# Kernel optimization log

Hardware: AMD Instinct MI355X
Metric: run time of the kernel (lower is better)

The kernel has to match this reference:

```python
import jax, jax.numpy as jnp
import numpy as np

N_NODES = 100000
N_EDGES = 1600000
IN_DIM = 128
HEADS = 8
NEG_SLOPE = 0.2  # PyG GATConv default


def _glorot(key, shape):
    fan_in, fan_out = shape[0], shape[-1]
    lim = jnp.sqrt(6.0 / (fan_in + fan_out))
    return jax.random.uniform(key, shape, jnp.float32, -lim, lim)


def setup_inputs() -> dict:
    key = jax.random.key(0)
    ks = jax.random.split(key, 20)
    x = jax.random.normal(ks[0], (N_NODES, IN_DIM), jnp.float32)
    edge_index = jax.random.randint(ks[1], (2, N_EDGES), 0, N_NODES, jnp.int32)
    # layer 1: 128 -> 8 heads x 16
    W1 = _glorot(ks[2], (128, 128)); a_src1 = _glorot(ks[3], (8, 16)); a_dst1 = _glorot(ks[4], (8, 16)); b1 = jnp.zeros((128,), jnp.float32)
    # layer 2: 128 -> 8 heads x 16
    W2 = _glorot(ks[5], (128, 128)); a_src2 = _glorot(ks[6], (8, 16)); a_dst2 = _glorot(ks[7], (8, 16)); b2 = jnp.zeros((128,), jnp.float32)
    # layer 3: 128 -> 1 head x 64, concat=False (mean)
    W3 = _glorot(ks[8], (128, 64)); a_src3 = _glorot(ks[9], (1, 64)); a_dst3 = _glorot(ks[10], (1, 64)); b3 = jnp.zeros((64,), jnp.float32)
    Wout = _glorot(ks[11], (64, 2)); bout = jnp.zeros((2,), jnp.float32)
    return {"x": x, "edge_index": edge_index,
            "W1": W1, "a_src1": a_src1, "a_dst1": a_dst1, "b1": b1,
            "W2": W2, "a_src2": a_src2, "a_dst2": a_dst2, "b2": b2,
            "W3": W3, "a_src3": a_src3, "a_dst3": a_dst3, "b3": b3,
            "Wout": Wout, "bout": bout}


def gat_conv(x, src, dst, W, a_src, a_dst, bias, concat):
    """PyG-style GATConv (eval mode, self-loops already appended to src/dst)."""
    n = x.shape[0]
    H, C = a_src.shape
    h = (x @ W).reshape(n, H, C)                        # [N,H,C]
    alpha_src = jnp.einsum('nhc,hc->nh', h, a_src)       # [N,H]
    alpha_dst = jnp.einsum('nhc,hc->nh', h, a_dst)       # [N,H]
    e = jax.nn.leaky_relu(alpha_src[src] + alpha_dst[dst], NEG_SLOPE)  # [E,H]
    # segment softmax over incoming edges of each destination node
    m = jax.ops.segment_max(e, dst, num_segments=n)      # [N,H]
    ex = jnp.exp(e - m[dst])
    denom = jax.ops.segment_sum(ex, dst, num_segments=n)  # [N,H]
    alpha = ex / (denom[dst] + 1e-16)                    # [E,H]
    # weighted gather-scatter aggregation
    msg = alpha[:, :, None] * h[src]                     # [E,H,C]
    out = jax.ops.segment_sum(msg, dst, num_segments=n)  # [N,H,C]
    out = out.reshape(n, H * C) if concat else out.mean(axis=1)
    return out + bias


def reference(x, edge_index, W1, a_src1, a_dst1, b1, W2, a_src2, a_dst2, b2,
              W3, a_src3, a_dst3, b3, Wout, bout):
    n = x.shape[0]
    loops = jnp.arange(n, dtype=edge_index.dtype)
    src = jnp.concatenate([edge_index[0], loops])
    dst = jnp.concatenate([edge_index[1], loops])
    h = jax.nn.elu(gat_conv(x, src, dst, W1, a_src1, a_dst1, b1, concat=True))
    h = jax.nn.elu(gat_conv(h, src, dst, W2, a_src2, a_dst2, b2, concat=True))
    h = jax.nn.elu(gat_conv(h, src, dst, W3, a_src3, a_dst3, b3, concat=False))
    return h @ Wout + bout
```

## Files before the change

### kernel.cpp

```cpp
#include <hip/hip_runtime.h>
#include <math.h>

#define NN 100000
#define NE 1600000
#define ET (NE + NN)
#define SCAN_BLK 4096

__device__ inline unsigned short f2bf(float f) {
  union { float f; unsigned u; } v; v.f = f;
  unsigned r = v.u + 0x7fffu + ((v.u >> 16) & 1u);
  return (unsigned short)(r >> 16);
}
__device__ inline float bflo(unsigned u) { union { unsigned u; float f; } v; v.u = u << 16; return v.f; }
__device__ inline float bfhi(unsigned u) { union { unsigned u; float f; } v; v.u = u & 0xffff0000u; return v.f; }

__global__ __launch_bounds__(256) void k_hist(const int* __restrict__ dst, int* __restrict__ counts,
                                              int* __restrict__ slots) {
  int base = blockIdx.x * 1024 + threadIdx.x;
#pragma unroll
  for (int j = 0; j < 4; ++j) {
    int i = base + j * 256;
    if (i < ET) {
      int d = (i < NE) ? dst[i] : (i - NE);
      slots[i] = atomicAdd(&counts[d], 1);
    }
  }
}

__global__ __launch_bounds__(256) void k_scan1(const int* __restrict__ counts, int* __restrict__ partial,
                                               int* __restrict__ blksum) {
  __shared__ int lds[256];
  int b = blockIdx.x, t = threadIdx.x;
  int base = b * SCAN_BLK + t * 16;
  int v[16];
  int s = 0;
#pragma unroll
  for (int j = 0; j < 16; j++) {
    int x = (base + j < NN) ? counts[base + j] : 0;
    s += x; v[j] = s;
  }
  lds[t] = s; __syncthreads();
  int tot = s;
  for (int off = 1; off < 256; off <<= 1) {
    int u = 0; if (t >= off) u = lds[t - off];
    __syncthreads(); lds[t] += u; __syncthreads();
  }
  int pre = lds[t] - tot;
#pragma unroll
  for (int j = 0; j < 16; j++) if (base + j < NN) partial[base + j] = pre + v[j];
  if (t == 255) blksum[b] = lds[255];
}

__global__ __launch_bounds__(256) void k_scan2(int* __restrict__ blksum, int nb) {
  __shared__ int lds[256];
  int t = threadIdx.x;
  int v = (t < nb) ? blksum[t] : 0;
  lds[t] = v; __syncthreads();
  for (int off = 1; off < 256; off <<= 1) {
    int u = 0; if (t >= off) u = lds[t - off];
    __syncthreads(); lds[t] += u; __syncthreads();
  }
  if (t < nb) blksum[t] = lds[t] - v;
}

__global__ __launch_bounds__(256) void k_scan3(const int* __restrict__ partial, const int* __restrict__ blksum,
                                               int* __restrict__ rowptr) {
  int i = blockIdx.x * 256 + threadIdx.x;
  if (i >= NN) return;
  rowptr[i + 1] = partial[i] + blksum[i / SCAN_BLK];
  if (i == 0) rowptr[0] = 0;
}

__global__ __launch_bounds__(256) void k_scatter(const int* __restrict__ src, const int* __restrict__ dst,
                                                 const int* __restrict__ rowptr, const int* __restrict__ slots,
                                                 int* __restrict__ esrc) {
  int base = blockIdx.x * 1024 + threadIdx.x;
#pragma unroll
  for (int j = 0; j < 4; ++j) {
    int i = base + j * 256;
    if (i < ET) {
      int d, s;
      if (i < NE) { d = dst[i]; s = src[i]; } else { d = i - NE; s = d; }
      esrc[rowptr[d] + slots[i]] = s;
    }
  }
}

template<int M, bool XBF>
__global__ __launch_bounds__(256) void k_gemm(const float* __restrict__ Xf, const unsigned short* __restrict__ Xb,
                                              const float* __restrict__ W,
                                              const float* __restrict__ a_src, const float* __restrict__ a_dst,
                                              unsigned short* __restrict__ Hf, float* __restrict__ as_, float* __restrict__ ad_) {
  constexpr int CPT = M / 16;
  __shared__ float xs[64 * 36];
  __shared__ float ws[32 * M];
  const int t = threadIdx.x;
  const int tx = t & 15, ty = t >> 4;
  const int row0 = blockIdx.x * 64;
  const int c0 = tx * CPT;
  float acc[4][CPT];
#pragma unroll
  for (int i = 0; i < 4; i++)
#pragma unroll
    for (int j = 0; j < CPT; j++) acc[i][j] = 0.f;

  for (int st = 0; st < 4; ++st) {
    const int k0 = st * 32;
    __syncthreads();
    if constexpr (!XBF) {
#pragma unroll
      for (int j = 0; j < 2; ++j) {
        int flat = t + j * 256;
        int r = flat >> 3, c4 = (flat & 7) * 4;
        float4 v = make_float4(0.f, 0.f, 0.f, 0.f);
        if (row0 + r < NN) v = *(const float4*)(Xf + (size_t)(row0 + r) * 128 + k0 + c4);
        *(float4*)(xs + r * 36 + c4) = v;
      }
    } else {
      int r = t >> 2, c8 = (t & 3) * 8;
      uint4 v = make_uint4(0, 0, 0, 0);
      if (row0 + r < NN) v = *(const uint4*)(Xb + (size_t)(row0 + r) * 128 + k0 + c8);
      float* d = xs + r * 36 + c8;
      d[0] = bflo(v.x); d[1] = bfhi(v.x); d[2] = bflo(v.y); d[3] = bfhi(v.y);
      d[4] = bflo(v.z); d[5] = bfhi(v.z); d[6] = bflo(v.w); d[7] = bfhi(v.w);
    }
#pragma unroll
    for (int j = 0; j < M / 32; ++j) {
      int flat = t + j * 256;
      int r = flat / (M / 4), c4 = (flat % (M / 4)) * 4;
      *(float4*)(ws + r * M + c4) = *(const float4*)(W + (size_t)(k0 + r) * M + c4);
    }
    __syncthreads();
#pragma unroll
    for (int kk = 0; kk < 32; kk += 4) {
      float4 xv[4];
#pragma unroll
      for (int i = 0; i < 4; ++i) xv[i] = *(const float4*)(xs + (ty * 4 + i) * 36 + kk);
#pragma unroll
      for (int j = 0; j < 4; ++j) {
#pragma unroll
        for (int cc = 0; cc < CPT; cc += 4) {
          float4 wv = *(const float4*)(ws + (kk + j) * M + c0 + cc);
#pragma unroll
          for (int i = 0; i < 4; ++i) {
            float xx = ((const float*)&xv[i])[j];
            acc[i][cc + 0] += xx * wv.x;
            acc[i][cc + 1] += xx * wv.y;
            acc[i][cc + 2] += xx * wv.z;
            acc[i][cc + 3] += xx * wv.w;
          }
        }
      }
    }
  }

  float s1[4], s2[4];
#pragma unroll
  for (int i = 0; i < 4; ++i) {
    float a = 0.f, b = 0.f;
#pragma unroll
    for (int j = 0; j < CPT; ++j) { a += acc[i][j] * a_src[c0 + j]; b += acc[i][j] * a_dst[c0 + j]; }
    s1[i] = a; s2[i] = b;
  }
  if constexpr (M == 128) {
#pragma unroll
    for (int i = 0; i < 4; ++i) { s1[i] += __shfl_xor(s1[i], 1); s2[i] += __shfl_xor(s2[i], 1); }
  } else {
#pragma unroll
    for (int off = 1; off < 16; off <<= 1)
#pragma unroll
      for (int i = 0; i < 4; ++i) { s1[i] += __shfl_xor(s1[i], off); s2[i] += __shfl_xor(s2[i], off); }
  }
#pragma unroll
  for (int i = 0; i < 4; ++i) {
    int r = row0 + ty * 4 + i;
    if (r < NN) {
      if constexpr (M == 128) {
        uint4 pk;
        pk.x = (unsigned)f2bf(acc[i][0]) | ((unsigned)f2bf(acc[i][1]) << 16);
        pk.y = (unsigned)f2bf(acc[i][2]) | ((unsigned)f2bf(acc[i][3]) << 16);
        pk.z = (unsigned)f2bf(acc[i][4]) | ((unsigned)f2bf(acc[i][5]) << 16);
        pk.w = (unsigned)f2bf(acc[i][6]) | ((unsigned)f2bf(acc[i][7]) << 16);
        *(uint4*)(Hf + (size_t)r * M + c0) = pk;
        if ((tx & 1) == 0) { as_[r * 8 + (tx >> 1)] = s1[i]; ad_[r * 8 + (tx >> 1)] = s2[i]; }
      } else {
        uint2 pk;
        pk.x = (unsigned)f2bf(acc[i][0]) | ((unsigned)f2bf(acc[i][1]) << 16);
        pk.y = (unsigned)f2bf(acc[i][2]) | ((unsigned)f2bf(acc[i][3]) << 16);
        *(uint2*)(Hf + (size_t)r * M + c0) = pk;
        if (tx == 0) { as_[r] = s1[i]; ad_[r] = s2[i]; }
      }
    }
  }
}

template<int HH, int C, bool FINAL>
__global__ __launch_bounds__(256) void k_aggregate(const unsigned short* __restrict__ Hf,
                                                   const float* __restrict__ as_, const float* __restrict__ ad_,
                                                   const int* __restrict__ rowptr, const int* __restrict__ esrc,
                                                   const float* __restrict__ bias,
                                                   const float* __restrict__ Wout, const float* __restrict__ bout,
                                                   unsigned short* __restrict__ outb, float* __restrict__ outf) {
  constexpr int CT = HH * C;
  constexpr int Q = CT / 8;
  int g = blockIdx.x * 256 + threadIdx.x;
  if (g >= NN * Q) return;
  int node = g / Q;
  int q = g - node * Q;
  int c = q * 8;
  int hh = c / C;
  int i0 = rowptr[node], i1 = rowptr[node + 1];
  float ad = ad_[node * HH + hh];
  float d0 = 0.f, d1 = 0.f;
  float a0[8], a1[8];
#pragma unroll
  for (int j = 0; j < 8; ++j) { a0[j] = 0.f; a1[j] = 0.f; }
  int i = i0;
  for (; i + 1 < i1; i += 2) {
    int sA = esrc[i], sB = esrc[i + 1];
    float eA = as_[sA * HH + hh] + ad;
    float eB = as_[sB * HH + hh] + ad;
    uint4 hA = *(const uint4*)(Hf + (size_t)sA * CT + c);
    uint4 hB = *(const uint4*)(Hf + (size_t)sB * CT + c);
    eA = fmaxf(eA, 0.2f * eA);
    eB = fmaxf(eB, 0.2f * eB);
    float pA = __expf(eA), pB = __expf(eB);
    d0 += pA;                             d1 += pB;
    a0[0] = fmaf(pA, bflo(hA.x), a0[0]);  a1[0] = fmaf(pB, bflo(hB.x), a1[0]);
    a0[1] = fmaf(pA, bfhi(hA.x), a0[1]);  a1[1] = fmaf(pB, bfhi(hB.x), a1[1]);
    a0[2] = fmaf(pA, bflo(hA.y), a0[2]);  a1[2] = fmaf(pB, bflo(hB.y), a1[2]);
    a0[3] = fmaf(pA, bfhi(hA.y), a0[3]);  a1[3] = fmaf(pB, bfhi(hB.y), a1[3]);
    a0[4] = fmaf(pA, bflo(hA.z), a0[4]);  a1[4] = fmaf(pB, bflo(hB.z), a1[4]);
    a0[5] = fmaf(pA, bfhi(hA.z), a0[5]);  a1[5] = fmaf(pB, bfhi(hB.z), a1[5]);
    a0[6] = fmaf(pA, bflo(hA.w), a0[6]);  a1[6] = fmaf(pB, bflo(hB.w), a1[6]);
    a0[7] = fmaf(pA, bfhi(hA.w), a0[7]);  a1[7] = fmaf(pB, bfhi(hB.w), a1[7]);
  }
  if (i < i1) {
    int sA = esrc[i];
    float eA = as_[sA * HH + hh] + ad;
    uint4 hA = *(const uint4*)(Hf + (size_t)sA * CT + c);
    eA = fmaxf(eA, 0.2f * eA);
    float pA = __expf(eA);
    d0 += pA;
    a0[0] = fmaf(pA, bflo(hA.x), a0[0]);
    a0[1] = fmaf(pA, bfhi(hA.x), a0[1]);
    a0[2] = fmaf(pA, bflo(hA.y), a0[2]);
    a0[3] = fmaf(pA, bfhi(hA.y), a0[3]);
    a0[4] = fmaf(pA, bflo(hA.z), a0[4]);
    a0[5] = fmaf(pA, bfhi(hA.z), a0[5]);
    a0[6] = fmaf(pA, bflo(hA.w), a0[6]);
    a0[7] = fmaf(pA, bfhi(hA.w), a0[7]);
  }
  float inv = 1.f / (d0 + d1);
  float o[8];
#pragma unroll
  for (int j = 0; j < 8; ++j) {
    float v = (a0[j] + a1[j]) * inv + bias[c + j];
    o[j] = v > 0.f ? v : __expf(v) - 1.f;
  }
  if constexpr (!FINAL) {
    uint4 pk;
    pk.x = (unsigned)f2bf(o[0]) | ((unsigned)f2bf(o[1]) << 16);
    pk.y = (unsigned)f2bf(o[2]) | ((unsigned)f2bf(o[3]) << 16);
    pk.z = (unsigned)f2bf(o[4]) | ((unsigned)f2bf(o[5]) << 16);
    pk.w = (unsigned)f2bf(o[6]) | ((unsigned)f2bf(o[7]) << 16);
    *(uint4*)(outb + (size_t)node * CT + c) = pk;
  } else {
    float p0 = 0.f, p1 = 0.f;
#pragma unroll
    for (int j = 0; j < 8; ++j) { p0 += o[j] * Wout[(c + j) * 2 + 0]; p1 += o[j] * Wout[(c + j) * 2 + 1]; }
#pragma unroll
    for (int off = 1; off < 8; off <<= 1) { p0 += __shfl_xor(p0, off); p1 += __shfl_xor(p1, off); }
    if (q == 0) { outf[node * 2 + 0] = p0 + bout[0]; outf[node * 2 + 1] = p1 + bout[1]; }
  }
}

extern "C" void kernel_launch(void* const* d_in, const int* in_sizes, int n_in,
                              void* d_out, int out_size, void* d_ws, size_t ws_size,
                              hipStream_t stream) {
  const float* x    = (const float*)d_in[0];
  const int*   ei   = (const int*)d_in[1];
  const float* W1   = (const float*)d_in[2];
  const float* as1  = (const float*)d_in[3];
  const float* ad1  = (const float*)d_in[4];
  const float* b1   = (const float*)d_in[5];
  const float* W2   = (const float*)d_in[6];
  const float* as2  = (const float*)d_in[7];
  const float* ad2  = (const float*)d_in[8];
  const float* b2   = (const float*)d_in[9];
  const float* W3   = (const float*)d_in[10];
  const float* as3  = (const float*)d_in[11];
  const float* ad3  = (const float*)d_in[12];
  const float* b3   = (const float*)d_in[13];
  const float* Wout = (const float*)d_in[14];
  const float* bout = (const float*)d_in[15];
  const int* srcp = ei;
  const int* dstp = ei + NE;

  char* p = (char*)d_ws;
  auto alloc = [&](size_t bytes) { char* r = p; p += (bytes + 255) & ~size_t(255); return r; };
  int*            rowptr  = (int*)alloc((size_t)(NN + 1) * 4);
  int*            counts  = (int*)alloc((size_t)NN * 4);
  int*            partial = (int*)alloc((size_t)NN * 4);
  int*            blksum  = (int*)alloc(256 * 4);
  int*            esrc    = (int*)alloc((size_t)ET * 4);
  int*            slots   = (int*)alloc((size_t)ET * 4);
  float*          asb     = (float*)alloc((size_t)NN * 8 * 4);
  float*          adb     = (float*)alloc((size_t)NN * 8 * 4);
  unsigned short* hfb     = (unsigned short*)alloc((size_t)NN * 128 * 2);
  unsigned short* actb    = (unsigned short*)alloc((size_t)NN * 128 * 2);

  hipMemsetAsync(counts, 0, (size_t)NN * 4, stream);
  int gE4 = (ET + 1023) / 1024;
  int nb = (NN + SCAN_BLK - 1) / SCAN_BLK;
  k_hist<<<gE4, 256, 0, stream>>>(dstp, counts, slots);
  k_scan1<<<nb, 256, 0, stream>>>(counts, partial, blksum);
  k_scan2<<<1, 256, 0, stream>>>(blksum, nb);
  k_scan3<<<(NN + 255) / 256, 256, 0, stream>>>(partial, blksum, rowptr);
  k_scatter<<<gE4, 256, 0, stream>>>(srcp, dstp, rowptr, slots, esrc);

  int gGemm = (NN + 63) / 64;
  k_gemm<128, false><<<gGemm, 256, 0, stream>>>(x, nullptr, W1, as1, ad1, hfb, asb, adb);
  k_aggregate<8, 16, false><<<(NN * 16 + 255) / 256, 256, 0, stream>>>(hfb, asb, adb, rowptr, esrc, b1, nullptr, nullptr, actb, nullptr);
  k_gemm<128, true><<<gGemm, 256, 0, stream>>>(nullptr, actb, W2, as2, ad2, hfb, asb, adb);
  k_aggregate<8, 16, false><<<(NN * 16 + 255) / 256, 256, 0, stream>>>(hfb, asb, adb, rowptr, esrc, b2, nullptr, nullptr, actb, nullptr);
  k_gemm<64, true><<<gGemm, 256, 0, stream>>>(nullptr, actb, W3, as3, ad3, hfb, asb, adb);
  k_aggregate<1, 64, true><<<(NN * 8 + 255) / 256, 256, 0, stream>>>(hfb, asb, adb, rowptr, esrc, b3, Wout, bout, nullptr, (float*)d_out);
}
```

Before: 450.5 us.

## Use bf16 MFMA for GEMM, unroll aggregation by four, enlarge edge-kernel blocks

The node-feature GEMM is rewritten to use bf16 MFMA 16x16x32 instructions, with the input and a transposed copy of the weights staged in LDS as bf16. The attention dot products are computed from the LDS-staged bf16 output. The aggregation loop now processes four edges per iteration with separate accumulators to expose more memory-level parallelism. The histogram and scatter kernels each handle eight elements per thread instead of four. The GEMM now rounds the layer-1 input and all weights to bf16, which lowers precision, and the attention logits are computed from the rounded outputs.

```diff
diff --git a/kernel.cpp b/kernel.cpp
--- a/kernel.cpp
+++ b/kernel.cpp
@@ -6,6 +6,9 @@
 #define ET (NE + NN)
 #define SCAN_BLK 4096
 
+typedef __attribute__((ext_vector_type(8))) short bf16x8;
+typedef __attribute__((ext_vector_type(4))) float f32x4;
+
 __device__ inline unsigned short f2bf(float f) {
   union { float f; unsigned u; } v; v.f = f;
   unsigned r = v.u + 0x7fffu + ((v.u >> 16) & 1u);
@@ -13,12 +16,13 @@
 }
 __device__ inline float bflo(unsigned u) { union { unsigned u; float f; } v; v.u = u << 16; return v.f; }
 __device__ inline float bfhi(unsigned u) { union { unsigned u; float f; } v; v.u = u & 0xffff0000u; return v.f; }
+__device__ inline float bfs(unsigned short u) { union { unsigned u; float f; } v; v.u = ((unsigned)u) << 16; return v.f; }
 
 __global__ __launch_bounds__(256) void k_hist(const int* __restrict__ dst, int* __restrict__ counts,
                                               int* __restrict__ slots) {
-  int base = blockIdx.x * 1024 + threadIdx.x;
-#pragma unroll
-  for (int j = 0; j < 4; ++j) {
+  int base = blockIdx.x * 2048 + threadIdx.x;
+#pragma unroll
+  for (int j = 0; j < 8; ++j) {
     int i = base + j * 256;
     if (i < ET) {
       int d = (i < NE) ? dst[i] : (i - NE);
@@ -74,9 +78,9 @@
 __global__ __launch_bounds__(256) void k_scatter(const int* __restrict__ src, const int* __restrict__ dst,
                                                  const int* __restrict__ rowptr, const int* __restrict__ slots,
                                                  int* __restrict__ esrc) {
-  int base = blockIdx.x * 1024 + threadIdx.x;
-#pragma unroll
-  for (int j = 0; j < 4; ++j) {
+  int base = blockIdx.x * 2048 + threadIdx.x;
+#pragma unroll
+  for (int j = 0; j < 8; ++j) {
     int i = base + j * 256;
     if (i < ET) {
       int d, s;
@@ -91,105 +95,126 @@
                                               const float* __restrict__ W,
                                               const float* __restrict__ a_src, const float* __restrict__ a_dst,
                                               unsigned short* __restrict__ Hf, float* __restrict__ as_, float* __restrict__ ad_) {
-  constexpr int CPT = M / 16;
-  __shared__ float xs[64 * 36];
-  __shared__ float ws[32 * M];
+  constexpr int NCBW = M / 64;
+  __shared__ __attribute__((aligned(16))) unsigned short xs[64 * 136];
+  __shared__ __attribute__((aligned(16))) unsigned short wt[M * 136];
+  __shared__ float asl[M], adl[M];
   const int t = threadIdx.x;
-  const int tx = t & 15, ty = t >> 4;
+  const int wave = t >> 6, l = t & 63;
+  const int lr = l & 15, kg = l >> 4;
+  const int wc0 = wave * (M / 4);
   const int row0 = blockIdx.x * 64;
-  const int c0 = tx * CPT;
-  float acc[4][CPT];
-#pragma unroll
-  for (int i = 0; i < 4; i++)
-#pragma unroll
-    for (int j = 0; j < CPT; j++) acc[i][j] = 0.f;
-
-  for (int st = 0; st < 4; ++st) {
-    const int k0 = st * 32;
-    __syncthreads();
-    if constexpr (!XBF) {
-#pragma unroll
-      for (int j = 0; j < 2; ++j) {
-        int flat = t + j * 256;
-        int r = flat >> 3, c4 = (flat & 7) * 4;
-        float4 v = make_float4(0.f, 0.f, 0.f, 0.f);
-        if (row0 + r < NN) v = *(const float4*)(Xf + (size_t)(row0 + r) * 128 + k0 + c4);
-        *(float4*)(xs + r * 36 + c4) = v;
+
+  if constexpr (XBF) {
+#pragma unroll
+    for (int p = 0; p < 4; ++p) {
+      int f = p * 256 + t;
+      int row = f >> 4, ch = f & 15;
+      uint4 v = make_uint4(0, 0, 0, 0);
+      if (row0 + row < NN) v = *(const uint4*)(Xb + (size_t)(row0 + row) * 128 + ch * 8);
+      *(uint4*)(xs + row * 136 + ch * 8) = v;
+    }
+  } else {
+#pragma unroll
+    for (int p = 0; p < 8; ++p) {
+      int f = p * 256 + t;
+      int row = f >> 5, ch = f & 31;
+      float4 v = make_float4(0.f, 0.f, 0.f, 0.f);
+      if (row0 + row < NN) v = *(const float4*)(Xf + (size_t)(row0 + row) * 128 + ch * 4);
+      uint2 pk;
+      pk.x = (unsigned)f2bf(v.x) | ((unsigned)f2bf(v.y) << 16);
+      pk.y = (unsigned)f2bf(v.z) | ((unsigned)f2bf(v.w) << 16);
+      *(uint2*)(xs + row * 136 + ch * 4) = pk;
+    }
+  }
+#pragma unroll
+  for (int p = 0; p < M / 8; ++p) {
+    int f = p * 256 + t;
+    int k = f & 127, cg = f >> 7;
+    float4 v = *(const float4*)(W + (size_t)k * M + cg * 4);
+    wt[(cg * 4 + 0) * 136 + k] = f2bf(v.x);
+    wt[(cg * 4 + 1) * 136 + k] = f2bf(v.y);
+    wt[(cg * 4 + 2) * 136 + k] = f2bf(v.z);
+    wt[(cg * 4 + 3) * 136 + k] = f2bf(v.w);
+  }
+  if (t < M) { asl[t] = a_src[t]; adl[t] = a_dst[t]; }
+  __syncthreads();
+
+  f32x4 acc[4][NCBW];
+#pragma unroll
+  for (int rb = 0; rb < 4; ++rb)
+#pragma unroll
+    for (int cb = 0; cb < NCBW; ++cb) acc[rb][cb] = (f32x4){0.f, 0.f, 0.f, 0.f};
+#pragma unroll
+  for (int kb = 0; kb < 4; ++kb) {
+    bf16x8 af[4], bfr[NCBW];
+#pragma unroll
+    for (int rb = 0; rb < 4; ++rb)
+      af[rb] = *(const bf16x8*)(xs + (rb * 16 + lr) * 136 + kb * 32 + kg * 8);
+#pragma unroll
+    for (int cb = 0; cb < NCBW; ++cb)
+      bfr[cb] = *(const bf16x8*)(wt + (size_t)(wc0 + cb * 16 + lr) * 136 + kb * 32 + kg * 8);
+#pragma unroll
+    for (int rb = 0; rb < 4; ++rb)
+#pragma unroll
+      for (int cb = 0; cb < NCBW; ++cb)
+        acc[rb][cb] = __builtin_amdgcn_mfma_f32_16x16x32_bf16(af[rb], bfr[cb], acc[rb][cb], 0, 0, 0);
+  }
+
+  __syncthreads();
+#pragma unroll
+  for (int rb = 0; rb < 4; ++rb)
+#pragma unroll
+    for (int cb = 0; cb < NCBW; ++cb)
+#pragma unroll
+      for (int r = 0; r < 4; ++r) {
+        int row = rb * 16 + kg * 4 + r;
+        int col = wc0 + cb * 16 + lr;
+        xs[row * 136 + col] = f2bf(acc[rb][cb][r]);
       }
-    } else {
-      int r = t >> 2, c8 = (t & 3) * 8;
-      uint4 v = make_uint4(0, 0, 0, 0);
-      if (row0 + r < NN) v = *(const uint4*)(Xb + (size_t)(row0 + r) * 128 + k0 + c8);
-      float* d = xs + r * 36 + c8;
-      d[0] = bflo(v.x); d[1] = bfhi(v.x); d[2] = bflo(v.y); d[3] = bfhi(v.y);
-      d[4] = bflo(v.z); d[5] = bfhi(v.z); d[6] = bflo(v.w); d[7] = bfhi(v.w);
-    }
-#pragma unroll
-    for (int j = 0; j < M / 32; ++j) {
-      int flat = t + j * 256;
-      int r = flat / (M / 4), c4 = (flat % (M / 4)) * 4;
-      *(float4*)(ws + r * M + c4) = *(const float4*)(W + (size_t)(k0 + r) * M + c4);
-    }
-    __syncthreads();
-#pragma unroll
-    for (int kk = 0; kk < 32; kk += 4) {
-      float4 xv[4];
-#pragma unroll
-      for (int i = 0; i < 4; ++i) xv[i] = *(const float4*)(xs + (ty * 4 + i) * 36 + kk);
-#pragma unroll
-      for (int j = 0; j < 4; ++j) {
-#pragma unroll
-        for (int cc = 0; cc < CPT; cc += 4) {
-          float4 wv = *(const float4*)(ws + (kk + j) * M + c0 + cc);
-#pragma unroll
-          for (int i = 0; i < 4; ++i) {
-            float xx = ((const float*)&xv[i])[j];
-            acc[i][cc + 0] += xx * wv.x;
-            acc[i][cc + 1] += xx * wv.y;
-            acc[i][cc + 2] += xx * wv.z;
-            acc[i][cc + 3] += xx * wv.w;
-          }
-        }
+  __syncthreads();
+
+  if constexpr (M == 128) {
+    int row = t >> 2, cg = t & 3;
+    int gr = row0 + row;
+    if (gr < NN) {
+#pragma unroll
+      for (int j = 0; j < 4; ++j)
+        *(uint4*)(Hf + (size_t)gr * 128 + cg * 32 + j * 8) = *(const uint4*)(xs + row * 136 + cg * 32 + j * 8);
+#pragma unroll
+      for (int hi = 0; hi < 2; ++hi) {
+        int hh = cg * 2 + hi;
+        uint4 u0 = *(const uint4*)(xs + row * 136 + hh * 16);
+        uint4 u1 = *(const uint4*)(xs + row * 136 + hh * 16 + 8);
+        float hv[16] = {bflo(u0.x), bfhi(u0.x), bflo(u0.y), bfhi(u0.y),
+                        bflo(u0.z), bfhi(u0.z), bflo(u0.w), bfhi(u0.w),
+                        bflo(u1.x), bfhi(u1.x), bflo(u1.y), bfhi(u1.y),
+                        bflo(u1.z), bfhi(u1.z), bflo(u1.w), bfhi(u1.w)};
+        float s1 = 0.f, s2 = 0.f;
+#pragma unroll
+        for (int j = 0; j < 16; ++j) { s1 += hv[j] * asl[hh * 16 + j]; s2 += hv[j] * adl[hh * 16 + j]; }
+        as_[(size_t)gr * 8 + hh] = s1;
+        ad_[(size_t)gr * 8 + hh] = s2;
       }
     }
-  }
-
-  float s1[4], s2[4];
-#pragma unroll
-  for (int i = 0; i < 4; ++i) {
-    float a = 0.f, b = 0.f;
-#pragma unroll
-    for (int j = 0; j < CPT; ++j) { a += acc[i][j] * a_src[c0 + j]; b += acc[i][j] * a_dst[c0 + j]; }
-    s1[i] = a; s2[i] = b;
-  }
-  if constexpr (M == 128) {
-#pragma unroll
-    for (int i = 0; i < 4; ++i) { s1[i] += __shfl_xor(s1[i], 1); s2[i] += __shfl_xor(s2[i], 1); }
   } else {
-#pragma unroll
-    for (int off = 1; off < 16; off <<= 1)
-#pragma unroll
-      for (int i = 0; i < 4; ++i) { s1[i] += __shfl_xor(s1[i], off); s2[i] += __shfl_xor(s2[i], off); }
-  }
-#pragma unroll
-  for (int i = 0; i < 4; ++i) {
-    int r = row0 + ty * 4 + i;
-    if (r < NN) {
-      if constexpr (M == 128) {
-        uint4 pk;
-        pk.x = (unsigned)f2bf(acc[i][0]) | ((unsigned)f2bf(acc[i][1]) << 16);
-        pk.y = (unsigned)f2bf(acc[i][2]) | ((unsigned)f2bf(acc[i][3]) << 16);
-        pk.z = (unsigned)f2bf(acc[i][4]) | ((unsigned)f2bf(acc[i][5]) << 16);
-        pk.w = (unsigned)f2bf(acc[i][6]) | ((unsigned)f2bf(acc[i][7]) << 16);
-        *(uint4*)(Hf + (size_t)r * M + c0) = pk;
-        if ((tx & 1) == 0) { as_[r * 8 + (tx >> 1)] = s1[i]; ad_[r * 8 + (tx >> 1)] = s2[i]; }
-      } else {
-        uint2 pk;
-        pk.x = (unsigned)f2bf(acc[i][0]) | ((unsigned)f2bf(acc[i][1]) << 16);
-        pk.y = (unsigned)f2bf(acc[i][2]) | ((unsigned)f2bf(acc[i][3]) << 16);
-        *(uint2*)(Hf + (size_t)r * M + c0) = pk;
-        if (tx == 0) { as_[r] = s1[i]; ad_[r] = s2[i]; }
-      }
+    int row = t >> 2, q = t & 3;
+    int gr = row0 + row;
+    uint4 u0 = *(const uint4*)(xs + row * 136 + q * 16);
+    uint4 u1 = *(const uint4*)(xs + row * 136 + q * 16 + 8);
+    float hv[16] = {bflo(u0.x), bfhi(u0.x), bflo(u0.y), bfhi(u0.y),
+                    bflo(u0.z), bfhi(u0.z), bflo(u0.w), bfhi(u0.w),
+                    bflo(u1.x), bfhi(u1.x), bflo(u1.y), bfhi(u1.y),
+                    bflo(u1.z), bfhi(u1.z), bflo(u1.w), bfhi(u1.w)};
+    float s1 = 0.f, s2 = 0.f;
+#pragma unroll
+    for (int j = 0; j < 16; ++j) { s1 += hv[j] * asl[q * 16 + j]; s2 += hv[j] * adl[q * 16 + j]; }
+    s1 += __shfl_xor(s1, 1); s1 += __shfl_xor(s1, 2);
+    s2 += __shfl_xor(s2, 1); s2 += __shfl_xor(s2, 2);
+    if (gr < NN) {
+      *(uint4*)(Hf + (size_t)gr * 64 + q * 16)     = u0;
+      *(uint4*)(Hf + (size_t)gr * 64 + q * 16 + 8) = u1;
+      if (q == 0) { as_[gr] = s1; ad_[gr] = s2; }
     }
   }
 }
@@ -211,51 +236,53 @@
   int hh = c / C;
   int i0 = rowptr[node], i1 = rowptr[node + 1];
   float ad = ad_[node * HH + hh];
-  float d0 = 0.f, d1 = 0.f;
-  float a0[8], a1[8];
-#pragma unroll
-  for (int j = 0; j < 8; ++j) { a0[j] = 0.f; a1[j] = 0.f; }
+  float d[4] = {0.f, 0.f, 0.f, 0.f};
+  float a[4][8] = {};
   int i = i0;
-  for (; i + 1 < i1; i += 2) {
-    int sA = esrc[i], sB = esrc[i + 1];
-    float eA = as_[sA * HH + hh] + ad;
-    float eB = as_[sB * HH + hh] + ad;
-    uint4 hA = *(const uint4*)(Hf + (size_t)sA * CT + c);
-    uint4 hB = *(const uint4*)(Hf + (size_t)sB * CT + c);
-    eA = fmaxf(eA, 0.2f * eA);
-    eB = fmaxf(eB, 0.2f * eB);
-    float pA = __expf(eA), pB = __expf(eB);
-    d0 += pA;                             d1 += pB;
-    a0[0] = fmaf(pA, bflo(hA.x), a0[0]);  a1[0] = fmaf(pB, bflo(hB.x), a1[0]);
-    a0[1] = fmaf(pA, bfhi(hA.x), a0[1]);  a1[1] = fmaf(pB, bfhi(hB.x), a1[1]);
-    a0[2] = fmaf(pA, bflo(hA.y), a0[2]);  a1[2] = fmaf(pB, bflo(hB.y), a1[2]);
-    a0[3] = fmaf(pA, bfhi(hA.y), a0[3]);  a1[3] = fmaf(pB, bfhi(hB.y), a1[3]);
-    a0[4] = fmaf(pA, bflo(hA.z), a0[4]);  a1[4] = fmaf(pB, bflo(hB.z), a1[4]);
-    a0[5] = fmaf(pA, bfhi(hA.z), a0[5]);  a1[5] = fmaf(pB, bfhi(hB.z), a1[5]);
-    a0[6] = fmaf(pA, bflo(hA.w), a0[6]);  a1[6] = fmaf(pB, bflo(hB.w), a1[6]);
-    a0[7] = fmaf(pA, bfhi(hA.w), a0[7]);  a1[7] = fmaf(pB, bfhi(hB.w), a1[7]);
-  }
-  if (i < i1) {
-    int sA = esrc[i];
-    float eA = as_[sA * HH + hh] + ad;
-    uint4 hA = *(const uint4*)(Hf + (size_t)sA * CT + c);
-    eA = fmaxf(eA, 0.2f * eA);
-    float pA = __expf(eA);
-    d0 += pA;
-    a0[0] = fmaf(pA, bflo(hA.x), a0[0]);
-    a0[1] = fmaf(pA, bfhi(hA.x), a0[1]);
-    a0[2] = fmaf(pA, bflo(hA.y), a0[2]);
-    a0[3] = fmaf(pA, bfhi(hA.y), a0[3]);
-    a0[4] = fmaf(pA, bflo(hA.z), a0[4]);
-    a0[5] = fmaf(pA, bfhi(hA.z), a0[5]);
-    a0[6] = fmaf(pA, bflo(hA.w), a0[6]);
-    a0[7] = fmaf(pA, bfhi(hA.w), a0[7]);
-  }
-  float inv = 1.f / (d0 + d1);
+  for (; i + 3 < i1; i += 4) {
+    int sx[4]; float ex[4]; uint4 hx[4];
+#pragma unroll
+    for (int c4 = 0; c4 < 4; ++c4) sx[c4] = esrc[i + c4];
+#pragma unroll
+    for (int c4 = 0; c4 < 4; ++c4) ex[c4] = as_[sx[c4] * HH + hh] + ad;
+#pragma unroll
+    for (int c4 = 0; c4 < 4; ++c4) hx[c4] = *(const uint4*)(Hf + (size_t)sx[c4] * CT + c);
+#pragma unroll
+    for (int c4 = 0; c4 < 4; ++c4) {
+      float e = fmaxf(ex[c4], 0.2f * ex[c4]);
+      float pp = __expf(e);
+      d[c4] += pp;
+      a[c4][0] = fmaf(pp, bflo(hx[c4].x), a[c4][0]);
+      a[c4][1] = fmaf(pp, bfhi(hx[c4].x), a[c4][1]);
+      a[c4][2] = fmaf(pp, bflo(hx[c4].y), a[c4][2]);
+      a[c4][3] = fmaf(pp, bfhi(hx[c4].y), a[c4][3]);
+      a[c4][4] = fmaf(pp, bflo(hx[c4].z), a[c4][4]);
+      a[c4][5] = fmaf(pp, bfhi(hx[c4].z), a[c4][5]);
+      a[c4][6] = fmaf(pp, bflo(hx[c4].w), a[c4][6]);
+      a[c4][7] = fmaf(pp, bfhi(hx[c4].w), a[c4][7]);
+    }
+  }
+  for (; i < i1; ++i) {
+    int s = esrc[i];
+    float e = as_[s * HH + hh] + ad;
+    uint4 h0 = *(const uint4*)(Hf + (size_t)s * CT + c);
+    e = fmaxf(e, 0.2f * e);
+    float pp = __expf(e);
+    d[0] += pp;
+    a[0][0] = fmaf(pp, bflo(h0.x), a[0][0]);
+    a[0][1] = fmaf(pp, bfhi(h0.x), a[0][1]);
+    a[0][2] = fmaf(pp, bflo(h0.y), a[0][2]);
+    a[0][3] = fmaf(pp, bfhi(h0.y), a[0][3]);
+    a[0][4] = fmaf(pp, bflo(h0.z), a[0][4]);
+    a[0][5] = fmaf(pp, bfhi(h0.z), a[0][5]);
+    a[0][6] = fmaf(pp, bflo(h0.w), a[0][6]);
+    a[0][7] = fmaf(pp, bfhi(h0.w), a[0][7]);
+  }
+  float inv = 1.f / (d[0] + d[1] + d[2] + d[3]);
   float o[8];
 #pragma unroll
   for (int j = 0; j < 8; ++j) {
-    float v = (a0[j] + a1[j]) * inv + bias[c + j];
+    float v = (a[0][j] + a[1][j] + a[2][j] + a[3][j]) * inv + bias[c + j];
     o[j] = v > 0.f ? v : __expf(v) - 1.f;
   }
   if constexpr (!FINAL) {
@@ -311,13 +338,13 @@
   unsigned short* actb    = (unsigned short*)alloc((size_t)NN * 128 * 2);
 
   hipMemsetAsync(counts, 0, (size_t)NN * 4, stream);
-  int gE4 = (ET + 1023) / 1024;
+  int gE8 = (ET + 2047) / 2048;
   int nb = (NN + SCAN_BLK - 1) / SCAN_BLK;
-  k_hist<<<gE4, 256, 0, stream>>>(dstp, counts, slots);
+  k_hist<<<gE8, 256, 0, stream>>>(dstp, counts, slots);
   k_scan1<<<nb, 256, 0, stream>>>(counts, partial, blksum);
   k_scan2<<<1, 256, 0, stream>>>(blksum, nb);
   k_scan3<<<(NN + 255) / 256, 256, 0, stream>>>(partial, blksum, rowptr);
-  k_scatter<<<gE4, 256, 0, stream>>>(srcp, dstp, rowptr, slots, esrc);
+  k_scatter<<<gE8, 256, 0, stream>>>(srcp, dstp, rowptr, slots, esrc);
 
   int gGemm = (NN + 63) / 64;
   k_gemm<128, false><<<gGemm, 256, 0, stream>>>(x, nullptr, W1, as1, ad1, hfb, asb, adb);
```

After: 388.9 us. 13.7% less time.
